# Performance work log

Measured on AMD Instinct MI355X. Metric: run time of the kernel, lower is better.

Reference implementation:

```python
import jax, jax.numpy as jnp
import numpy as np

N = 100000   # nodes
E = 3200000  # edges
D = 16       # n_qubits / feature dim
H = 64       # classifier hidden
C = 10       # output_dims
L = 2        # len(q_depths)


def setup_inputs() -> dict:
    key = jax.random.key(0)
    ks = jax.random.split(key, 16)
    s = 1.0 / np.sqrt(D)
    return {
        "x": jax.random.normal(ks[0], (N, D), jnp.float32),
        "edge_index": jax.random.randint(ks[1], (2, E), 0, N, dtype=jnp.int32),
        "edge_attr": jax.random.uniform(ks[2], (E,), jnp.float32),
        "batch": jnp.zeros((N,), jnp.int32),
        # per-layer GCNConv params
        "lin_w": jax.random.uniform(ks[3], (L, D, D), jnp.float32, -s, s),
        "conv_b": jnp.zeros((L, D), jnp.float32),
        # per-layer nodeNN (stand-in for quantum_net): tanh(W x + b)
        "node_w": jax.random.uniform(ks[4], (L, D, D), jnp.float32, -s, s),
        "node_b": jnp.zeros((L, D), jnp.float32),
        # per-layer LayerNorm affine
        "ln_g": jnp.ones((L, D), jnp.float32),
        "ln_b": jnp.zeros((L, D), jnp.float32),
        # classifier
        "w1": jax.random.normal(ks[5], (H, D), jnp.float32) * np.sqrt(2.0 / (D + H)),
        "b1": jnp.zeros((H,), jnp.float32),
        "w2": jax.random.normal(ks[6], (C, H), jnp.float32) * np.sqrt(2.0 / (H + C)),
        "b2": jnp.zeros((C,), jnp.float32),
    }


def _layer_norm(h, g, b, eps=1e-5):
    mu = h.mean(-1, keepdims=True)
    var = ((h - mu) ** 2).mean(-1, keepdims=True)
    return (h - mu) * jax.lax.rsqrt(var + eps) * g + b


def reference(x, edge_index, edge_attr, batch, lin_w, conv_b, node_w, node_b,
              ln_g, ln_b, w1, b1, w2, b2):
    n = x.shape[0]
    # gcn_norm with add_self_loops=True (fill_value=1)
    loop = jnp.arange(n, dtype=edge_index.dtype)
    row = jnp.concatenate([edge_index[0], loop])  # source
    col = jnp.concatenate([edge_index[1], loop])  # target
    ew = jnp.concatenate([edge_attr, jnp.ones((n,), x.dtype)])
    deg = jax.ops.segment_sum(ew, col, num_segments=n)
    dinv = jnp.where(deg > 0, jax.lax.rsqrt(jnp.maximum(deg, 1e-30)), 0.0)
    norm = dinv[row] * ew * dinv[col]  # [E+N]

    h = x
    n_layers = lin_w.shape[0]
    for i in range(n_layers):
        out = h @ lin_w[i].T                      # lin (no bias)
        msg = norm[:, None] * out[row]            # gather + scale, [E+N, D]
        agg = jax.ops.segment_sum(msg, col, num_segments=n)  # scatter-add
        out = jnp.tanh(agg @ node_w[i].T + node_b[i])  # nodeNN update (quantum_net stand-in)
        out = out + conv_b[i]
        h = jnp.where(out > 0, out, 0.2 * out)    # LeakyReLU(0.2)
        h = _layer_norm(h, ln_g[i], ln_b[i])

    h = jax.nn.relu(h @ w1.T + b1)                # classifier (dropout = identity at eval)
    return h @ w2.T + b2
```

## Files before the change

### kernel.cpp

```cpp
#include <hip/hip_runtime.h>
#include <hip/hip_bf16.h>

namespace {

constexpr int N_NODES = 100000;
constexpr int N_EDGES = 3200000;
constexpr int D = 16;
constexpr int H = 64;
constexpr int C = 10;
constexpr int L = 2;
constexpr int BLK = 256;
constexpr int BLKS = 512;
constexpr int NBN = (N_NODES + BLK - 1) / BLK;

constexpr int P = 64;
constexpr int NP = (N_NODES + P - 1) / P;

constexpr int CBN = 256;
constexpr int NC = (N_NODES + CBN - 1) / CBN;
constexpr int NPTR = NC * CBN + 1;

constexpr int NBB = 1024;
constexpr int EC = N_EDGES / NBB;
constexpr int REC2_CAP = N_EDGES + 7 * N_NODES;

__device__ inline unsigned short f2bf(float f) {
  unsigned u = __float_as_uint(f);
  return (unsigned short)((u + 0x7FFFu + ((u >> 16) & 1u)) >> 16);
}
__device__ inline float bf2f(unsigned short b) {
  return __uint_as_float(((unsigned)b) << 16);
}

__global__ void k_bincount(const int* __restrict__ col, int* __restrict__ blk_hist) {
  __shared__ int lh[NC];
  for (int i = threadIdx.x; i < NC; i += BLKS) lh[i] = 0;
  __syncthreads();
  const int b = blockIdx.x;
  const int e0 = b * EC, e1 = e0 + EC;
  for (int e = e0 + threadIdx.x; e < e1; e += 4 * BLKS) {
    int cc[4]; bool ok[4];
#pragma unroll
    for (int j = 0; j < 4; ++j) {
      int ee = e + j * BLKS;
      ok[j] = ee < e1;
      cc[j] = ok[j] ? col[ee] : 0;
    }
#pragma unroll
    for (int j = 0; j < 4; ++j)
      if (ok[j]) atomicAdd(&lh[cc[j] >> 8], 1);
  }
  __syncthreads();
  for (int i = threadIdx.x; i < NC; i += BLKS)
    blk_hist[(size_t)b * NC + i] = lh[i];
}

__global__ void k_colscan(int* __restrict__ blk_hist, int* __restrict__ bin_cnt) {
  const int i = blockIdx.x;
  const int t = threadIdx.x;
  int v[4];
  int s = 0;
#pragma unroll
  for (int j = 0; j < 4; ++j) {
    v[j] = blk_hist[(size_t)(t * 4 + j) * NC + i];
    s += v[j];
  }
  const int lane = t & 63;
  int incl = s;
#pragma unroll
  for (int off = 1; off < 64; off <<= 1) {
    int y = __shfl_up(incl, off, 64);
    if (lane >= off) incl += y;
  }
  __shared__ int wsum[4];
  const int w = t >> 6;
  if (lane == 63) wsum[w] = incl;
  __syncthreads();
  int wbase = 0;
#pragma unroll
  for (int k = 0; k < 4; ++k) wbase += (k < w) ? wsum[k] : 0;
  int excl = wbase + incl - s;
#pragma unroll
  for (int j = 0; j < 4; ++j) {
    blk_hist[(size_t)(t * 4 + j) * NC + i] = excl;
    excl += v[j];
  }
  if (t == BLK - 1) bin_cnt[i] = excl;
}

__global__ void k_scan(const int* __restrict__ src, int* __restrict__ dst, int n,
                       int sentinel) {
  __shared__ int s0[2048], s1[2048];
  const int t = threadIdx.x;
  int v0 = (t < n) ? src[t] : 0;
  int v1 = (t + 1024 < n) ? src[t + 1024] : 0;
  s0[t] = v0; s0[t + 1024] = v1;
  __syncthreads();
  int* cur = s0; int* nxt = s1;
  for (int off = 1; off < 2048; off <<= 1) {
    nxt[t] = cur[t] + (t >= off ? cur[t - off] : 0);
    int i1 = t + 1024;
    nxt[i1] = cur[i1] + (i1 >= off ? cur[i1 - off] : 0);
    __syncthreads();
    int* tmp = cur; cur = nxt; nxt = tmp;
  }
  if (t < n) dst[t] = cur[t] - v0;
  if (t + 1024 < n) dst[t + 1024] = cur[t + 1024] - v1;
  if (t == 0 && sentinel >= 0) dst[n] = sentinel;
}

__global__ void k_binscatter(const int* __restrict__ row, const int* __restrict__ col,
                             const float* __restrict__ ew, const int* __restrict__ coarse_ptr,
                             const int* __restrict__ blk_hist, uint2* __restrict__ recs) {
  __shared__ int lcur[NC];
  const int b = blockIdx.x;
  for (int i = threadIdx.x; i < NC; i += BLKS)
    lcur[i] = coarse_ptr[i] + blk_hist[(size_t)b * NC + i];
  __syncthreads();
  const int e0 = b * EC, e1 = e0 + EC;
  for (int e = e0 + threadIdx.x; e < e1; e += 4 * BLKS) {
    int cc[4], rr[4]; float ww[4]; bool ok[4];
#pragma unroll
    for (int j = 0; j < 4; ++j) {
      int ee = e + j * BLKS;
      ok[j] = ee < e1;
      cc[j] = ok[j] ? col[ee] : 0;
      rr[j] = ok[j] ? row[ee] : 0;
      ww[j] = ok[j] ? ew[ee] : 0.f;
    }
#pragma unroll
    for (int j = 0; j < 4; ++j) {
      if (ok[j]) {
        int c = cc[j];
        int pos = atomicAdd(&lcur[c >> 8], 1);
        recs[pos] = make_uint2((unsigned)rr[j] | ((unsigned)(c & (CBN - 1)) << 17),
                               __float_as_uint(ww[j]));
      }
    }
  }
}

__global__ void k_cntnode(const uint2* __restrict__ recs, const int* __restrict__ coarse_ptr,
                          int* __restrict__ cnt_g, int* __restrict__ pad_cnt) {
  __shared__ int cnt[CBN];
  __shared__ int ws[4];
  const int b = blockIdx.x;
  const int tid = threadIdx.x;
  if (tid < CBN) cnt[tid] = 0;
  __syncthreads();
  const int beg = coarse_ptr[b], end = coarse_ptr[b + 1];
  for (int p = beg + tid; p < end; p += 4 * BLKS) {
    unsigned xx[4]; bool ok[4];
#pragma unroll
    for (int j = 0; j < 4; ++j) {
      int pp = p + j * BLKS;
      ok[j] = pp < end;
      xx[j] = ok[j] ? recs[pp].x : 0u;
    }
#pragma unroll
    for (int j = 0; j < 4; ++j)
      if (ok[j]) atomicAdd(&cnt[xx[j] >> 17], 1);
  }
  __syncthreads();
  if (tid < CBN) {
    int c = cnt[tid];
    cnt_g[b * CBN + tid] = c;
    int pv = (c + 7) & ~7;
#pragma unroll
    for (int m = 1; m < 64; m <<= 1) pv += __shfl_xor(pv, m, 64);
    if ((tid & 63) == 0) ws[tid >> 6] = pv;
  }
  __syncthreads();
  if (tid == 0) pad_cnt[b] = ws[0] + ws[1] + ws[2] + ws[3];
}

__global__ void k_sortscatter(const uint2* __restrict__ recs, const int* __restrict__ coarse_ptr,
                              const int* __restrict__ cnt_g, const int* __restrict__ pad_ptr,
                              int* __restrict__ node_ptr, uint2* __restrict__ recs2) {
  __shared__ int cur[CBN];
  __shared__ int fin[CBN];
  __shared__ int wsum[4];
  const int b = blockIdx.x;
  const int tid = threadIdx.x;
  int pc = 0, incl = 0;
  if (tid < CBN) {
    pc = (cnt_g[b * CBN + tid] + 7) & ~7;
    incl = pc;
    const int lane = tid & 63;
#pragma unroll
    for (int off = 1; off < 64; off <<= 1) {
      int y = __shfl_up(incl, off, 64);
      if (lane >= off) incl += y;
    }
    if (lane == 63) wsum[tid >> 6] = incl;
  }
  __syncthreads();
  if (tid < CBN) {
    const int w = tid >> 6;
    int wb = 0;
#pragma unroll
    for (int k = 0; k < 4; ++k) wb += (k < w) ? wsum[k] : 0;
    int excl = wb + incl - pc + pad_ptr[b];
    cur[tid] = excl;
    fin[tid] = excl + pc;
    node_ptr[b * CBN + tid] = excl;
    if (b == NC - 1 && tid == CBN - 1) node_ptr[NC * CBN] = excl + pc;
  }
  __syncthreads();
  const int beg = coarse_ptr[b], end = coarse_ptr[b + 1];
  for (int p = beg + tid; p < end; p += 4 * BLKS) {
    uint2 r[4]; bool ok[4];
#pragma unroll
    for (int j = 0; j < 4; ++j) {
      int pp = p + j * BLKS;
      ok[j] = pp < end;
      r[j] = ok[j] ? recs[pp] : make_uint2(0u, 0u);
    }
#pragma unroll
    for (int j = 0; j < 4; ++j) {
      if (ok[j]) {
        int pos = atomicAdd(&cur[r[j].x >> 17], 1);
        recs2[pos] = make_uint2(r[j].x & 0x1FFFF, r[j].y);
      }
    }
  }
  __syncthreads();
  if (tid < CBN) {
    for (int q = cur[tid]; q < fin[tid]; ++q) recs2[q] = make_uint2(0u, 0u);
  }
}

__global__ void k_dinv2(const int* __restrict__ node_ptr, const uint2* __restrict__ recs2,
                        float* __restrict__ dinv) {
  int v = blockIdx.x * BLK + threadIdx.x;
  if (v >= N_NODES) return;
  float s = 1.0f;
  int e = node_ptr[v + 1];
  for (int p = node_ptr[v]; p < e; ++p) s += __uint_as_float(recs2[p].y);
  dinv[v] = s > 0.f ? rsqrtf(fmaxf(s, 1e-30f)) : 0.f;
}

__global__ void k_lin(const float* __restrict__ hin, const float* __restrict__ W,
                      const float* __restrict__ dinv, unsigned short* __restrict__ outd) {
  __shared__ float sW[D * D];
  sW[threadIdx.x] = W[threadIdx.x];
  __syncthreads();
  int v = blockIdx.x * BLK + threadIdx.x;
  if (v >= N_NODES) return;
  float hv[D];
  const float4* hp = reinterpret_cast<const float4*>(hin + (size_t)v * D);
#pragma unroll
  for (int c = 0; c < 4; ++c) {
    float4 t = hp[c];
    hv[4 * c + 0] = t.x; hv[4 * c + 1] = t.y;
    hv[4 * c + 2] = t.z; hv[4 * c + 3] = t.w;
  }
  float dv = dinv[v];
  unsigned short ob[D];
#pragma unroll
  for (int j = 0; j < D; ++j) {
    float s = 0.f;
#pragma unroll
    for (int k = 0; k < D; ++k) s += hv[k] * sW[j * D + k];
    ob[j] = f2bf(s * dv);
  }
  uint4 w0, w1;
  w0.x = (unsigned)ob[0]  | ((unsigned)ob[1]  << 16);
  w0.y = (unsigned)ob[2]  | ((unsigned)ob[3]  << 16);
  w0.z = (unsigned)ob[4]  | ((unsigned)ob[5]  << 16);
  w0.w = (unsigned)ob[6]  | ((unsigned)ob[7]  << 16);
  w1.x = (unsigned)ob[8]  | ((unsigned)ob[9]  << 16);
  w1.y = (unsigned)ob[10] | ((unsigned)ob[11] << 16);
  w1.z = (unsigned)ob[12] | ((unsigned)ob[13] << 16);
  w1.w = (unsigned)ob[14] | ((unsigned)ob[15] << 16);
  uint4* op = reinterpret_cast<uint4*>(outd + (size_t)v * D);
  op[0] = w0;
  op[1] = w1;
}

__global__ void k_agg(const int* __restrict__ node_ptr, const uint2* __restrict__ recs2,
                      const float* __restrict__ dinv, const unsigned short* __restrict__ outd,
                      const float* __restrict__ Wn, const float* __restrict__ nb,
                      const float* __restrict__ cb, const float* __restrict__ lg,
                      const float* __restrict__ lb, float* __restrict__ h) {
  __shared__ float sacc[P * 17];
  __shared__ float sdinv[P];
  __shared__ float sWT[D * D];
  __shared__ float snb[D], scb[D], slg[D], slb[D];
  const int b = blockIdx.x;
  const int base = b * P;
  const int tid = threadIdx.x;

  sWT[tid] = Wn[(tid & 15) * D + (tid >> 4)];
  if (tid < D) {
    snb[tid] = nb[tid]; scb[tid] = cb[tid];
    slg[tid] = lg[tid]; slb[tid] = lb[tid];
  }
  if (tid < P) {
    int v = base + tid;
    sdinv[tid] = (v < N_NODES) ? dinv[v] : 0.f;
  }

  const int g = tid >> 4;
  const int l = tid & 15;
#pragma unroll
  for (int i = 0; i < P / 16; ++i) {
    const int n = g + 16 * i;
    const int v = base + n;
    float acc = (v < N_NODES) ? bf2f(outd[(size_t)v * D + l]) : 0.f;
    int p = node_ptr[v];
    const int e = node_ptr[v + 1];
    for (; p < e; p += 8) {
      const uint4* rp = reinterpret_cast<const uint4*>(recs2 + p);
      uint4 q0 = rp[0], q1 = rp[1], q2 = rp[2], q3 = rp[3];
      float g0 = bf2f(outd[(size_t)q0.x * D + l]);
      float g1 = bf2f(outd[(size_t)q0.z * D + l]);
      float g2 = bf2f(outd[(size_t)q1.x * D + l]);
      float g3 = bf2f(outd[(size_t)q1.z * D + l]);
      float g4 = bf2f(outd[(size_t)q2.x * D + l]);
      float g5 = bf2f(outd[(size_t)q2.z * D + l]);
      float g6 = bf2f(outd[(size_t)q3.x * D + l]);
      float g7 = bf2f(outd[(size_t)q3.z * D + l]);
      acc = fmaf(__uint_as_float(q0.y), g0, acc);
      acc = fmaf(__uint_as_float(q0.w), g1, acc);
      acc = fmaf(__uint_as_float(q1.y), g2, acc);
      acc = fmaf(__uint_as_float(q1.w), g3, acc);
      acc = fmaf(__uint_as_float(q2.y), g4, acc);
      acc = fmaf(__uint_as_float(q2.w), g5, acc);
      acc = fmaf(__uint_as_float(q3.y), g6, acc);
      acc = fmaf(__uint_as_float(q3.w), g7, acc);
    }
    sacc[n * 17 + l] = acc;
  }
  __syncthreads();

#pragma unroll
  for (int nb0 = 0; nb0 < P / 16; ++nb0) {
    int n = nb0 * 16 + g;
    int v = base + n;
    float s = 0.f;
#pragma unroll
    for (int k = 0; k < D; ++k) s += sacc[n * 17 + k] * sWT[k * D + l];
    s = snb[l] + sdinv[n] * s;
    float u = tanhf(s) + scb[l];
    u = u > 0.f ? u : 0.2f * u;
    float mu = u;
#pragma unroll
    for (int m = 1; m < 16; m <<= 1) mu += __shfl_xor(mu, m, 64);
    mu *= (1.0f / D);
    float dd = u - mu;
    float var = dd * dd;
#pragma unroll
    for (int m = 1; m < 16; m <<= 1) var += __shfl_xor(var, m, 64);
    var *= (1.0f / D);
    float inv = rsqrtf(var + 1e-5f);
    if (v < N_NODES) h[(size_t)v * D + l] = dd * inv * slg[l] + slb[l];
  }
}

__global__ void k_cls(const float* __restrict__ h, const float* __restrict__ w1,
                      const float* __restrict__ b1, const float* __restrict__ w2,
                      const float* __restrict__ b2, float* __restrict__ out) {
  __shared__ float sw1[H * D];
  __shared__ float sb1[H];
  __shared__ float sw2[C * H];
  __shared__ float sb2[C];
  for (int i = threadIdx.x; i < H * D; i += BLK) sw1[i] = w1[i];
  for (int i = threadIdx.x; i < H; i += BLK) sb1[i] = b1[i];
  for (int i = threadIdx.x; i < C * H; i += BLK) sw2[i] = w2[i];
  for (int i = threadIdx.x; i < C; i += BLK) sb2[i] = b2[i];
  __syncthreads();
  int v = blockIdx.x * BLK + threadIdx.x;
  if (v >= N_NODES) return;
  float hv[D];
  const float4* hp = reinterpret_cast<const float4*>(h + (size_t)v * D);
#pragma unroll
  for (int c = 0; c < 4; ++c) {
    float4 t = hp[c];
    hv[4 * c + 0] = t.x; hv[4 * c + 1] = t.y;
    hv[4 * c + 2] = t.z; hv[4 * c + 3] = t.w;
  }
  float oc[C];
#pragma unroll
  for (int c = 0; c < C; ++c) oc[c] = sb2[c];
#pragma unroll
  for (int j = 0; j < H; ++j) {
    float s = sb1[j];
#pragma unroll
    for (int k = 0; k < D; ++k) s += hv[k] * sw1[j * D + k];
    s = fmaxf(s, 0.f);
#pragma unroll
    for (int c = 0; c < C; ++c) oc[c] += s * sw2[c * H + j];
  }
#pragma unroll
  for (int c = 0; c < C; ++c) out[(size_t)v * C + c] = oc[c];
}

inline char* align_up(char* p, size_t a) {
  return (char*)(((uintptr_t)p + a - 1) & ~(uintptr_t)(a - 1));
}

}

extern "C" void kernel_launch(void* const* d_in, const int* in_sizes, int n_in,
                              void* d_out, int out_size, void* d_ws, size_t ws_size,
                              hipStream_t stream) {
  const float* x         = (const float*)d_in[0];
  const int*   edge_idx  = (const int*)d_in[1];
  const float* edge_attr = (const float*)d_in[2];
  const float* lin_w  = (const float*)d_in[4];
  const float* conv_b = (const float*)d_in[5];
  const float* node_w = (const float*)d_in[6];
  const float* node_b = (const float*)d_in[7];
  const float* ln_g   = (const float*)d_in[8];
  const float* ln_b   = (const float*)d_in[9];
  const float* w1     = (const float*)d_in[10];
  const float* b1     = (const float*)d_in[11];
  const float* w2     = (const float*)d_in[12];
  const float* b2     = (const float*)d_in[13];
  float* out = (float*)d_out;

  const int* row = edge_idx;
  const int* col = edge_idx + N_EDGES;

  char* p = (char*)d_ws;
  int*   bin_cnt    = (int*)p;   p = align_up(p + sizeof(int) * NC, 256);
  int*   coarse_ptr = (int*)p;   p = align_up(p + sizeof(int) * (NC + 1), 256);
  int*   pad_cnt    = (int*)p;   p = align_up(p + sizeof(int) * NC, 256);
  int*   pad_ptr    = (int*)p;   p = align_up(p + sizeof(int) * (NC + 1), 256);
  int*   cnt_g      = (int*)p;   p = align_up(p + sizeof(int) * (size_t)(NC * CBN), 256);
  int*   node_ptr   = (int*)p;   p = align_up(p + sizeof(int) * (size_t)NPTR, 256);
  float* dinv       = (float*)p; p = align_up(p + sizeof(float) * N_NODES, 256);
  char*  recs_mem   = p;         p = align_up(p + sizeof(uint2) * (size_t)N_EDGES, 256);
  uint2* recs2      = (uint2*)p; p = align_up(p + sizeof(uint2) * (size_t)REC2_CAP, 256);

  uint2* recs = (uint2*)recs_mem;
  unsigned short* outb = (unsigned short*)recs_mem;
  float* hbuf = (float*)align_up(recs_mem + sizeof(unsigned short) * (size_t)N_NODES * D, 256);
  int*   blk_hist = (int*)recs2;

  k_bincount<<<NBB, BLKS, 0, stream>>>(col, blk_hist);
  k_colscan<<<NC, BLK, 0, stream>>>(blk_hist, bin_cnt);
  k_scan<<<1, 1024, 0, stream>>>(bin_cnt, coarse_ptr, NC, N_EDGES);
  k_binscatter<<<NBB, BLKS, 0, stream>>>(row, col, edge_attr, coarse_ptr, blk_hist, recs);
  k_cntnode<<<NC, BLKS, 0, stream>>>(recs, coarse_ptr, cnt_g, pad_cnt);
  k_scan<<<1, 1024, 0, stream>>>(pad_cnt, pad_ptr, NC, -1);
  k_sortscatter<<<NC, BLKS, 0, stream>>>(recs, coarse_ptr, cnt_g, pad_ptr, node_ptr, recs2);
  k_dinv2<<<NBN, BLK, 0, stream>>>(node_ptr, recs2, dinv);

  for (int i = 0; i < L; ++i) {
    const float* hin = (i == 0) ? x : hbuf;
    k_lin<<<NBN, BLK, 0, stream>>>(hin, lin_w + i * D * D, dinv, outb);
    k_agg<<<NP, BLK, 0, stream>>>(node_ptr, recs2, dinv, outb,
                                  node_w + i * D * D, node_b + i * D, conv_b + i * D,
                                  ln_g + i * D, ln_b + i * D, hbuf);
  }
  k_cls<<<NBN, BLK, 0, stream>>>(hbuf, w1, b1, w2, b2, out);
}
```

Baseline: 206.9 us.

## Prefetch next edge-record batch in aggregation and shrink per-block node tile

The aggregation kernel now software-pipelines its edge-record loads: the next 8 records are fetched while the current 8 gathers and FMAs run, so record-load latency overlaps with the gather chain. Nodes per block drop from 64 to 32, doubling the grid to spread uneven-degree work across more blocks. The bin-scatter kernel is unrolled from 4 to 8 edges per thread to keep more loads in flight. Costs are more registers per thread, which may lower occupancy, and a redundant reload of the last batch on the final iteration.

New measurement: 194.5 us. 6.0% less time.

```diff
diff --git a/kernel.cpp b/kernel.cpp
--- a/kernel.cpp
+++ b/kernel.cpp
@@ -13,8 +13,8 @@
 constexpr int BLKS = 512;
 constexpr int NBN = (N_NODES + BLK - 1) / BLK;
 
-constexpr int P = 64;
-constexpr int NP = (N_NODES + P - 1) / P;
+constexpr int PA = 32;
+constexpr int NP = (N_NODES + PA - 1) / PA;
 
 constexpr int CBN = 256;
 constexpr int NC = (N_NODES + CBN - 1) / CBN;
@@ -118,10 +118,10 @@
     lcur[i] = coarse_ptr[i] + blk_hist[(size_t)b * NC + i];
   __syncthreads();
   const int e0 = b * EC, e1 = e0 + EC;
-  for (int e = e0 + threadIdx.x; e < e1; e += 4 * BLKS) {
-    int cc[4], rr[4]; float ww[4]; bool ok[4];
-#pragma unroll
-    for (int j = 0; j < 4; ++j) {
+  for (int e = e0 + threadIdx.x; e < e1; e += 8 * BLKS) {
+    int cc[8], rr[8]; float ww[8]; bool ok[8];
+#pragma unroll
+    for (int j = 0; j < 8; ++j) {
       int ee = e + j * BLKS;
       ok[j] = ee < e1;
       cc[j] = ok[j] ? col[ee] : 0;
@@ -129,7 +129,7 @@
       ww[j] = ok[j] ? ew[ee] : 0.f;
     }
 #pragma unroll
-    for (int j = 0; j < 4; ++j) {
+    for (int j = 0; j < 8; ++j) {
       if (ok[j]) {
         int c = cc[j];
         int pos = atomicAdd(&lcur[c >> 8], 1);
@@ -283,12 +283,12 @@
                       const float* __restrict__ Wn, const float* __restrict__ nb,
                       const float* __restrict__ cb, const float* __restrict__ lg,
                       const float* __restrict__ lb, float* __restrict__ h) {
-  __shared__ float sacc[P * 17];
-  __shared__ float sdinv[P];
+  __shared__ float sacc[PA * 17];
+  __shared__ float sdinv[PA];
   __shared__ float sWT[D * D];
   __shared__ float snb[D], scb[D], slg[D], slb[D];
   const int b = blockIdx.x;
-  const int base = b * P;
+  const int base = b * PA;
   const int tid = threadIdx.x;
 
   sWT[tid] = Wn[(tid & 15) * D + (tid >> 4)];
@@ -296,7 +296,7 @@
     snb[tid] = nb[tid]; scb[tid] = cb[tid];
     slg[tid] = lg[tid]; slb[tid] = lb[tid];
   }
-  if (tid < P) {
+  if (tid < PA) {
     int v = base + tid;
     sdinv[tid] = (v < N_NODES) ? dinv[v] : 0.f;
   }
@@ -304,38 +304,45 @@
   const int g = tid >> 4;
   const int l = tid & 15;
 #pragma unroll
-  for (int i = 0; i < P / 16; ++i) {
+  for (int i = 0; i < PA / 16; ++i) {
     const int n = g + 16 * i;
     const int v = base + n;
     float acc = (v < N_NODES) ? bf2f(outd[(size_t)v * D + l]) : 0.f;
     int p = node_ptr[v];
     const int e = node_ptr[v + 1];
+    uint4 a0, a1, a2, a3;
+    if (p < e) {
+      const uint4* rp = reinterpret_cast<const uint4*>(recs2 + p);
+      a0 = rp[0]; a1 = rp[1]; a2 = rp[2]; a3 = rp[3];
+    }
     for (; p < e; p += 8) {
-      const uint4* rp = reinterpret_cast<const uint4*>(recs2 + p);
-      uint4 q0 = rp[0], q1 = rp[1], q2 = rp[2], q3 = rp[3];
-      float g0 = bf2f(outd[(size_t)q0.x * D + l]);
-      float g1 = bf2f(outd[(size_t)q0.z * D + l]);
-      float g2 = bf2f(outd[(size_t)q1.x * D + l]);
-      float g3 = bf2f(outd[(size_t)q1.z * D + l]);
-      float g4 = bf2f(outd[(size_t)q2.x * D + l]);
-      float g5 = bf2f(outd[(size_t)q2.z * D + l]);
-      float g6 = bf2f(outd[(size_t)q3.x * D + l]);
-      float g7 = bf2f(outd[(size_t)q3.z * D + l]);
-      acc = fmaf(__uint_as_float(q0.y), g0, acc);
-      acc = fmaf(__uint_as_float(q0.w), g1, acc);
-      acc = fmaf(__uint_as_float(q1.y), g2, acc);
-      acc = fmaf(__uint_as_float(q1.w), g3, acc);
-      acc = fmaf(__uint_as_float(q2.y), g4, acc);
-      acc = fmaf(__uint_as_float(q2.w), g5, acc);
-      acc = fmaf(__uint_as_float(q3.y), g6, acc);
-      acc = fmaf(__uint_as_float(q3.w), g7, acc);
+      const int pn = (p + 8 < e) ? p + 8 : p;
+      const uint4* rpn = reinterpret_cast<const uint4*>(recs2 + pn);
+      uint4 b0 = rpn[0], b1 = rpn[1], b2 = rpn[2], b3 = rpn[3];
+      float g0 = bf2f(outd[(size_t)a0.x * D + l]);
+      float g1 = bf2f(outd[(size_t)a0.z * D + l]);
+      float g2 = bf2f(outd[(size_t)a1.x * D + l]);
+      float g3 = bf2f(outd[(size_t)a1.z * D + l]);
+      float g4 = bf2f(outd[(size_t)a2.x * D + l]);
+      float g5 = bf2f(outd[(size_t)a2.z * D + l]);
+      float g6 = bf2f(outd[(size_t)a3.x * D + l]);
+      float g7 = bf2f(outd[(size_t)a3.z * D + l]);
+      acc = fmaf(__uint_as_float(a0.y), g0, acc);
+      acc = fmaf(__uint_as_float(a0.w), g1, acc);
+      acc = fmaf(__uint_as_float(a1.y), g2, acc);
+      acc = fmaf(__uint_as_float(a1.w), g3, acc);
+      acc = fmaf(__uint_as_float(a2.y), g4, acc);
+      acc = fmaf(__uint_as_float(a2.w), g5, acc);
+      acc = fmaf(__uint_as_float(a3.y), g6, acc);
+      acc = fmaf(__uint_as_float(a3.w), g7, acc);
+      a0 = b0; a1 = b1; a2 = b2; a3 = b3;
     }
     sacc[n * 17 + l] = acc;
   }
   __syncthreads();
 
 #pragma unroll
-  for (int nb0 = 0; nb0 < P / 16; ++nb0) {
+  for (int nb0 = 0; nb0 < PA / 16; ++nb0) {
     int n = nb0 * 16 + g;
     int v = base + n;
     float s = 0.f;
```
